# Kernel optimization log

Hardware: AMD Instinct MI355X
Metric: run time of the kernel (lower is better)

The kernel has to match this reference:

```python
import jax, jax.numpy as jnp
import numpy as np

N = 100000      # nodes
E = 1600000     # edges
IN_C = 64       # in_channels
HID = 128       # hidden_channels
K = 2           # Chebyshev order
EPS = 1e-5      # BatchNorm eps
SLOPE = 0.01    # LeakyReLU negative slope


def _glorot(key, shape, fan_in):
    lim = 1.0 / np.sqrt(fan_in)
    return jax.random.uniform(key, shape, jnp.float32, -lim, lim)


def setup_inputs() -> dict:
    key = jax.random.key(0)
    ks = jax.random.split(key, 12)
    x = jax.random.normal(ks[0], (N, IN_C), jnp.float32)
    edge_index = jax.random.randint(ks[1], (2, E), 0, N, dtype=jnp.int32)
    # ChebConv weights: one [Cin, Cout] matrix per Chebyshev order, plus bias.
    W1 = _glorot(ks[2], (K, IN_C, HID), IN_C)
    b1 = _glorot(ks[3], (HID,), IN_C)
    W2 = _glorot(ks[4], (K, HID, HID // 2), HID)
    b2 = _glorot(ks[5], (HID // 2,), HID)
    W3 = _glorot(ks[6], (K, HID // 2, IN_C), HID // 2)
    b3 = _glorot(ks[7], (IN_C,), HID // 2)
    # BatchNorm affine params
    gamma1 = jnp.ones((HID,), jnp.float32)
    beta1 = jnp.zeros((HID,), jnp.float32)
    gamma2 = jnp.ones((HID // 2,), jnp.float32)
    beta2 = jnp.zeros((HID // 2,), jnp.float32)
    return {"x": x, "edge_index": edge_index, "W1": W1, "b1": b1,
            "W2": W2, "b2": b2, "W3": W3, "b3": b3,
            "gamma1": gamma1, "beta1": beta1, "gamma2": gamma2, "beta2": beta2}


def reference(x, edge_index, W1, b1, W2, b2, W3, b3, gamma1, beta1, gamma2, beta2):
    row, col = edge_index[0], edge_index[1]
    # Scaled Laplacian with lambda_max=2 (PyG default): L_hat = -D^{-1/2} A D^{-1/2}
    deg = jax.ops.segment_sum(jnp.ones(row.shape, x.dtype), row, num_segments=N)
    dinv = jnp.where(deg > 0, jax.lax.rsqrt(jnp.where(deg > 0, deg, 1.0)), 0.0)
    ew = -dinv[row] * dinv[col]                     # [E] edge weights of L_hat

    def prop(h):  # y = L_hat @ h ; gather from source, scatter to target
        return jax.ops.segment_sum(ew[:, None] * h[row], col, num_segments=N)

    def cheb_conv(h, W, b):  # K=2: Tx0 = h, Tx1 = L_hat @ h
        return h @ W[0] + prop(h) @ W[1] + b

    def batchnorm(h, g, b):  # training-mode BN over node dim, biased variance
        m = h.mean(axis=0)
        v = jnp.mean(jnp.square(h - m), axis=0)
        return g * (h - m) * jax.lax.rsqrt(v + EPS) + b

    def lrelu(h):
        return jnp.where(h >= 0, h, SLOPE * h)

    h = lrelu(batchnorm(cheb_conv(x, W1, b1), gamma1, beta1))
    h = lrelu(batchnorm(cheb_conv(h, W2, b2), gamma2, beta2))
    return cheb_conv(h, W3, b3)
```

## Files before the change

kernel.cpp:

```cpp
#include <hip/hip_runtime.h>

#define NN 100000
#define NE 1600000
constexpr float BN_EPS = 1e-5f;
constexpr float LRELU_SLOPE = 0.01f;
constexpr int SC_NB = (NN + 255) / 256;
constexpr int RSH = 13;
constexpr int RB = 1 << RSH;
constexpr int NR = (NN + RB - 1) / RB;
constexpr int SB = 8;
constexpr int CAP = 163840;
constexpr int PBLK = 400;
constexpr int PCHUNK = NE / PBLK;

__global__ __launch_bounds__(256) void k_part(const int* __restrict__ row,
                                              const int* __restrict__ col,
                                              int* __restrict__ colCnt,
                                              int* __restrict__ rowCnt,
                                              int2* __restrict__ colbuf,
                                              int* __restrict__ rowbuf) {
  __shared__ int cntc[NR], cntr[NR];
  const int tid = threadIdx.x;
  const int e0 = blockIdx.x * PCHUNK;
  if (tid < NR) { cntc[tid] = 0; cntr[tid] = 0; }
  __syncthreads();
  for (int i = tid; i < PCHUNK; i += 256) {
    atomicAdd(&cntc[col[e0 + i] >> RSH], 1);
    atomicAdd(&cntr[row[e0 + i] >> RSH], 1);
  }
  __syncthreads();
  if (tid < NR) {
    cntc[tid] = atomicAdd(&colCnt[tid], cntc[tid]);
  } else if (tid >= 64 && tid < 64 + NR) {
    const int b = tid - 64;
    cntr[b] = atomicAdd(&rowCnt[b], cntr[b]);
  }
  __syncthreads();
  for (int i = tid; i < PCHUNK; i += 256) {
    const int r = row[e0 + i];
    const int c = col[e0 + i];
    const int bc = c >> RSH;
    const int pc = atomicAdd(&cntc[bc], 1);
    colbuf[(size_t)bc * CAP + pc] = make_int2(r, c);
    const int br = r >> RSH;
    const int pr = atomicAdd(&cntr[br], 1);
    rowbuf[(size_t)br * CAP + pr] = r;
  }
}

__global__ __launch_bounds__(1024) void k_hist2(const int2* __restrict__ colbuf,
                                                const int* __restrict__ rowbuf,
                                                const int* __restrict__ colCnt,
                                                const int* __restrict__ rowCnt,
                                                int* __restrict__ PDc,
                                                int* __restrict__ PDd) {
  __shared__ int h[RB];
  const int tid = threadIdx.x;
  const int b = blockIdx.x, s = blockIdx.y, z = blockIdx.z;
  for (int i = tid; i < RB; i += 1024) h[i] = 0;
  __syncthreads();
  const int base = b << RSH;
  const int len = z ? rowCnt[b] : colCnt[b];
  const int sl = (len + SB - 1) / SB;
  const int st = s * sl;
  const int en = min(st + sl, len);
  if (z == 0) {
    const int2* cb = colbuf + (size_t)b * CAP;
    for (int i = st + tid; i < en; i += 1024)
      atomicAdd(&h[cb[i].y - base], 1);
  } else {
    const int* rb = rowbuf + (size_t)b * CAP;
    for (int i = st + tid; i < en; i += 1024)
      atomicAdd(&h[rb[i] - base], 1);
  }
  __syncthreads();
  int* pd = (z ? PDd : PDc) + ((size_t)b * SB + s) * RB;
  for (int i = tid; i < RB; i += 1024) pd[i] = h[i];
}

__global__ __launch_bounds__(256) void k_csrmid2(const int* __restrict__ PDc,
                                                 const int* __restrict__ PDd,
                                                 int* __restrict__ Bpart,
                                                 int* __restrict__ cnt,
                                                 float* __restrict__ dinv) {
  const int n = blockIdx.x * 256 + threadIdx.x;
  if (n >= NN) return;
  const int b = n >> RSH, o = n & (RB - 1);
  int run = 0, dsum = 0;
#pragma unroll
  for (int s = 0; s < SB; s++) {
    Bpart[(size_t)s * NN + n] = run;
    run += PDc[((size_t)b * SB + s) * RB + o];
    dsum += PDd[((size_t)b * SB + s) * RB + o];
  }
  cnt[n] = run;
  dinv[n] = dsum > 0 ? rsqrtf((float)dsum) : 0.0f;
}

__global__ __launch_bounds__(256) void k_scan_a(const int* __restrict__ cnt,
                                                int* __restrict__ bsum) {
  __shared__ int sh[256];
  const int tid = threadIdx.x;
  const int i = blockIdx.x * 256 + tid;
  sh[tid] = (i < NN) ? cnt[i] : 0;
  __syncthreads();
  for (int st = 128; st > 0; st >>= 1) {
    if (tid < st) sh[tid] += sh[tid + st];
    __syncthreads();
  }
  if (tid == 0) bsum[blockIdx.x] = sh[0];
}

__global__ __launch_bounds__(512) void k_scan_b(const int* __restrict__ bsum,
                                                int* __restrict__ boff) {
  __shared__ int sh[512];
  const int tid = threadIdx.x;
  const int v = (tid < SC_NB) ? bsum[tid] : 0;
  sh[tid] = v;
  __syncthreads();
  for (int off = 1; off < 512; off <<= 1) {
    int t = (tid >= off) ? sh[tid - off] : 0;
    __syncthreads();
    sh[tid] += t;
    __syncthreads();
  }
  if (tid < SC_NB) boff[tid] = sh[tid] - v;
}

__global__ __launch_bounds__(256) void k_scan_c(const int* __restrict__ cnt,
                                                const int* __restrict__ boff,
                                                int* __restrict__ ptr) {
  __shared__ int sh[256];
  const int tid = threadIdx.x;
  const int i = blockIdx.x * 256 + tid;
  const int v = (i < NN) ? cnt[i] : 0;
  sh[tid] = v;
  __syncthreads();
  for (int off = 1; off < 256; off <<= 1) {
    int t = (tid >= off) ? sh[tid - off] : 0;
    __syncthreads();
    sh[tid] += t;
    __syncthreads();
  }
  const int excl = sh[tid] - v + boff[blockIdx.x];
  if (i < NN) {
    ptr[i] = excl;
    if (i == NN - 1) ptr[NN] = excl + v;
  }
}

__global__ __launch_bounds__(1024) void k_fill4(const int2* __restrict__ colbuf,
                                                const int* __restrict__ colCnt,
                                                const int* __restrict__ ptr,
                                                const int* __restrict__ Bpart,
                                                int* __restrict__ eb) {
  __shared__ int cur[RB];
  const int tid = threadIdx.x;
  const int b = blockIdx.x, s = blockIdx.y;
  const int base = b << RSH;
  const int nmax = min(RB, NN - base);
  const int* bp = Bpart + (size_t)s * NN + base;
  for (int i = tid; i < nmax; i += 1024) cur[i] = ptr[base + i] + bp[i];
  __syncthreads();
  const int len = colCnt[b];
  const int sl = (len + SB - 1) / SB;
  const int st = s * sl;
  const int en = min(st + sl, len);
  const int2* cb = colbuf + (size_t)b * CAP;
  for (int i = st + tid; i < en; i += 1024) {
    const int2 rec = cb[i];
    const int pos = atomicAdd(&cur[rec.y - base], 1);
    eb[pos] = rec.x;
  }
}

__global__ __launch_bounds__(256) void k_scale(const float* __restrict__ x,
                                               const float* __restrict__ dinv,
                                               float* __restrict__ xs) {
  const size_t i = (size_t)blockIdx.x * 256 + threadIdx.x;
  const int n = (int)(i >> 4);
  float4 v = reinterpret_cast<const float4*>(x)[i];
  const float d = dinv[n];
  v.x *= d; v.y *= d; v.z *= d; v.w *= d;
  reinterpret_cast<float4*>(xs)[i] = v;
}

template <bool ADD>
__global__ __launch_bounds__(256) void k_prop64(const float* __restrict__ p,
                                                const int* __restrict__ eb,
                                                const int* __restrict__ ptr,
                                                const float* __restrict__ g,
                                                const float* __restrict__ dinv,
                                                float* __restrict__ out) {
  const int node = blockIdx.x * 16 + (threadIdx.x >> 4);
  const int lane = threadIdx.x & 15;
  if (node >= NN) return;
  const int b = ptr[node], e = ptr[node + 1];
  float4 a0 = make_float4(0.f, 0.f, 0.f, 0.f);
  float4 a1 = make_float4(0.f, 0.f, 0.f, 0.f);
  float4 a2 = make_float4(0.f, 0.f, 0.f, 0.f);
  float4 a3 = make_float4(0.f, 0.f, 0.f, 0.f);
  const float4* hp = reinterpret_cast<const float4*>(p) + lane;
  int j = b;
  for (; j + 4 <= e; j += 4) {
    const int s0 = eb[j], s1 = eb[j + 1], s2 = eb[j + 2], s3 = eb[j + 3];
    const float4 h0 = hp[(size_t)s0 * 16];
    const float4 h1 = hp[(size_t)s1 * 16];
    const float4 h2 = hp[(size_t)s2 * 16];
    const float4 h3 = hp[(size_t)s3 * 16];
    a0.x += h0.x; a0.y += h0.y; a0.z += h0.z; a0.w += h0.w;
    a1.x += h1.x; a1.y += h1.y; a1.z += h1.z; a1.w += h1.w;
    a2.x += h2.x; a2.y += h2.y; a2.z += h2.z; a2.w += h2.w;
    a3.x += h3.x; a3.y += h3.y; a3.z += h3.z; a3.w += h3.w;
  }
  for (; j + 2 <= e; j += 2) {
    const int s0 = eb[j], s1 = eb[j + 1];
    const float4 h0 = hp[(size_t)s0 * 16];
    const float4 h1 = hp[(size_t)s1 * 16];
    a0.x += h0.x; a0.y += h0.y; a0.z += h0.z; a0.w += h0.w;
    a1.x += h1.x; a1.y += h1.y; a1.z += h1.z; a1.w += h1.w;
  }
  if (j < e) {
    const float4 h0 = hp[(size_t)eb[j] * 16];
    a0.x += h0.x; a0.y += h0.y; a0.z += h0.z; a0.w += h0.w;
  }
  a0.x += a1.x + a2.x + a3.x;
  a0.y += a1.y + a2.y + a3.y;
  a0.z += a1.z + a2.z + a3.z;
  a0.w += a1.w + a2.w + a3.w;
  if (ADD) {
    const float dn = dinv[node];
    const float4 gv = reinterpret_cast<const float4*>(g)[(size_t)node * 16 + lane];
    a0.x = gv.x - dn * a0.x;
    a0.y = gv.y - dn * a0.y;
    a0.z = gv.z - dn * a0.z;
    a0.w = gv.w - dn * a0.w;
  }
  reinterpret_cast<float4*>(out)[(size_t)node * 16 + lane] = a0;
}

__global__ __launch_bounds__(512) void k_conv1(const float* __restrict__ x,
                                               const float* __restrict__ y,
                                               const float* __restrict__ dinv,
                                               const float* __restrict__ W,
                                               const float* __restrict__ bias,
                                               float* __restrict__ out) {
  __shared__ float XA[64][65];
  __shared__ float XY[64][65];
  const int tid = threadIdx.x;
  const int lane = tid & 63;
  const int wv = __builtin_amdgcn_readfirstlane(tid >> 6);
  const int n0 = blockIdx.x * 64;
  for (int idx = tid; idx < 1024; idx += 512) {
    const int n = idx >> 4, k4 = idx & 15;
    int node = n0 + n;
    if (node >= NN) node = NN - 1;
    const float4 av = *reinterpret_cast<const float4*>(x + (size_t)node * 64 + k4 * 4);
    float4 yv = *reinterpret_cast<const float4*>(y + (size_t)node * 64 + k4 * 4);
    const float dn = -dinv[node];
    yv.x *= dn; yv.y *= dn; yv.z *= dn; yv.w *= dn;
    float* da = &XA[n][k4 * 4];
    da[0] = av.x; da[1] = av.y; da[2] = av.z; da[3] = av.w;
    float* dy = &XY[n][k4 * 4];
    dy[0] = yv.x; dy[1] = yv.y; dy[2] = yv.z; dy[3] = yv.w;
  }
  __syncthreads();
  const int cw0 = wv * 16;
  const float* __restrict__ W0 = W + cw0;
  const float* __restrict__ W1 = W + 64 * 128 + cw0;
  float acc[16];
#pragma unroll
  for (int j = 0; j < 16; j++) acc[j] = 0.f;
#pragma unroll 4
  for (int k = 0; k < 64; k++) {
    const float a = XA[lane][k];
    const float b = XY[lane][k];
#pragma unroll
    for (int j = 0; j < 16; j++)
      acc[j] += a * W0[(size_t)k * 128 + j] + b * W1[(size_t)k * 128 + j];
  }
  const int node = n0 + lane;
  if (node < NN) {
#pragma unroll
    for (int j = 0; j < 16; j += 4) {
      float4 o = make_float4(acc[j] + bias[cw0 + j], acc[j + 1] + bias[cw0 + j + 1],
                             acc[j + 2] + bias[cw0 + j + 2], acc[j + 3] + bias[cw0 + j + 3]);
      *reinterpret_cast<float4*>(out + (size_t)node * 128 + cw0 + j) = o;
    }
  }
}

template <int Cin>
__global__ __launch_bounds__(512) void k_gemm_dual(const float* __restrict__ h,
                                                   const float* __restrict__ W,
                                                   const float* __restrict__ bias,
                                                   const float* __restrict__ scale,
                                                   const float* __restrict__ shift,
                                                   const float* __restrict__ dinv,
                                                   float* __restrict__ g,
                                                   float* __restrict__ p) {
  __shared__ float XA[64][Cin + 1];
  const int tid = threadIdx.x;
  const int lane = tid & 63;
  const int wv = __builtin_amdgcn_readfirstlane(tid >> 6);
  const int n0 = blockIdx.x * 64;
  constexpr int C4 = Cin / 4;
  for (int idx = tid; idx < 64 * C4; idx += 512) {
    const int n = idx / C4, k4 = idx % C4;
    int node = n0 + n;
    if (node >= NN) node = NN - 1;
    float4 v = *reinterpret_cast<const float4*>(h + (size_t)node * Cin + k4 * 4);
    const float4 sc = *reinterpret_cast<const float4*>(scale + k4 * 4);
    const float4 sh = *reinterpret_cast<const float4*>(shift + k4 * 4);
    v.x = sc.x * v.x + sh.x; v.y = sc.y * v.y + sh.y;
    v.z = sc.z * v.z + sh.z; v.w = sc.w * v.w + sh.w;
    v.x = v.x >= 0.f ? v.x : LRELU_SLOPE * v.x;
    v.y = v.y >= 0.f ? v.y : LRELU_SLOPE * v.y;
    v.z = v.z >= 0.f ? v.z : LRELU_SLOPE * v.z;
    v.w = v.w >= 0.f ? v.w : LRELU_SLOPE * v.w;
    float* d = &XA[n][k4 * 4];
    d[0] = v.x; d[1] = v.y; d[2] = v.z; d[3] = v.w;
  }
  __syncthreads();
  const int cw0 = wv * 8;
  const float* __restrict__ Wa = W + cw0;
  const float* __restrict__ Wb = W + Cin * 64 + cw0;
  float ag[8], ap[8];
#pragma unroll
  for (int j = 0; j < 8; j++) { ag[j] = 0.f; ap[j] = 0.f; }
#pragma unroll 4
  for (int k = 0; k < Cin; k++) {
    const float a = XA[lane][k];
#pragma unroll
    for (int j = 0; j < 8; j++) {
      ag[j] += a * Wa[(size_t)k * 64 + j];
      ap[j] += a * Wb[(size_t)k * 64 + j];
    }
  }
  const int node = n0 + lane;
  if (node < NN) {
    const float dn = dinv[node];
#pragma unroll
    for (int j = 0; j < 8; j += 4) {
      float4 og = make_float4(ag[j] + bias[cw0 + j], ag[j + 1] + bias[cw0 + j + 1],
                              ag[j + 2] + bias[cw0 + j + 2], ag[j + 3] + bias[cw0 + j + 3]);
      *reinterpret_cast<float4*>(g + (size_t)node * 64 + cw0 + j) = og;
      float4 op = make_float4(ap[j] * dn, ap[j + 1] * dn, ap[j + 2] * dn, ap[j + 3] * dn);
      *reinterpret_cast<float4*>(p + (size_t)node * 64 + cw0 + j) = op;
    }
  }
}

template <int C>
__global__ __launch_bounds__(256) void k_bnstats(const float* __restrict__ h,
                                                 float* __restrict__ bnsum,
                                                 float* __restrict__ bnsq) {
  constexpr int RPB = 256 / C;
  constexpr int ROWS = 256;
  const int c = threadIdx.x % C;
  const int g = threadIdx.x / C;
  const int r0 = blockIdx.x * ROWS + g;
  const int rend = min(blockIdx.x * ROWS + ROWS, NN);
  float s = 0.f, sq = 0.f;
  for (int r = r0; r < rend; r += RPB) {
    float v = h[(size_t)r * C + c];
    s += v;
    sq += v * v;
  }
  __shared__ float ss[256], sg[256];
  ss[threadIdx.x] = s;
  sg[threadIdx.x] = sq;
  __syncthreads();
  for (int st = 128; st >= C; st >>= 1) {
    if (threadIdx.x < st) {
      ss[threadIdx.x] += ss[threadIdx.x + st];
      sg[threadIdx.x] += sg[threadIdx.x + st];
    }
    __syncthreads();
  }
  if (threadIdx.x < C) {
    atomicAdd(&bnsum[threadIdx.x], ss[threadIdx.x]);
    atomicAdd(&bnsq[threadIdx.x], sg[threadIdx.x]);
  }
}

template <int C>
__global__ void k_bnfin(const float* __restrict__ bnsum, const float* __restrict__ bnsq,
                        const float* __restrict__ gamma, const float* __restrict__ beta,
                        float* __restrict__ scale, float* __restrict__ shift) {
  int c = threadIdx.x;
  if (c < C) {
    float mean = bnsum[c] * (1.0f / NN);
    float var = bnsq[c] * (1.0f / NN) - mean * mean;
    float sc = gamma[c] * rsqrtf(var + BN_EPS);
    scale[c] = sc;
    shift[c] = beta[c] - mean * sc;
  }
}

extern "C" void kernel_launch(void* const* d_in, const int* in_sizes, int n_in,
                              void* d_out, int out_size, void* d_ws, size_t ws_size,
                              hipStream_t stream) {
  const float* x   = (const float*)d_in[0];
  const int*   ei  = (const int*)d_in[1];
  const int*   row = ei;
  const int*   col = ei + NE;
  const float* W1  = (const float*)d_in[2];
  const float* b1  = (const float*)d_in[3];
  const float* W2  = (const float*)d_in[4];
  const float* b2  = (const float*)d_in[5];
  const float* W3  = (const float*)d_in[6];
  const float* b3  = (const float*)d_in[7];
  const float* g1  = (const float*)d_in[8];
  const float* be1 = (const float*)d_in[9];
  const float* g2w = (const float*)d_in[10];
  const float* be2 = (const float*)d_in[11];
  float* out = (float*)d_out;

  char* ws = (char*)d_ws;
  size_t off = 0;
  auto alloc = [&](size_t bytes) -> void* {
    void* p = ws + off;
    off = (off + bytes + 255) & ~(size_t)255;
    return p;
  };

  float* bnsum1 = (float*)alloc(128 * 4);
  float* bnsq1  = (float*)alloc(128 * 4);
  float* bnsum2 = (float*)alloc(64 * 4);
  float* bnsq2  = (float*)alloc(64 * 4);
  int*   colCnt = (int*)alloc(NR * 4);
  int*   rowCnt = (int*)alloc(NR * 4);
  const size_t zero_bytes = off;
  float* dinv   = (float*)alloc(NN * 4);
  int*   cnt    = (int*)alloc(NN * 4);
  int*   ptr    = (int*)alloc((NN + 1) * 4);
  int*   bsum   = (int*)alloc(SC_NB * 4);
  int*   boff   = (int*)alloc(SC_NB * 4);
  int*   eb     = (int*)alloc((size_t)NE * 4);
  float* scale1 = (float*)alloc(128 * 4);
  float* shift1 = (float*)alloc(128 * 4);
  float* scale2 = (float*)alloc(64 * 4);
  float* shift2 = (float*)alloc(64 * 4);
  float* bufA   = (float*)alloc((size_t)NN * 64 * 4);
  float* bufB   = (float*)alloc((size_t)NN * 128 * 4);
  float* bufC   = (float*)alloc((size_t)NN * 64 * 4);
  float* bufD   = (float*)alloc((size_t)NN * 64 * 4);

  int2* colbuf = (int2*)bufB;
  int*  rowbuf = (int*)(colbuf + (size_t)NR * CAP);
  int*  PDc    = (int*)bufC;
  int*  PDd    = PDc + (size_t)NR * SB * RB;
  int*  Bpart  = PDd + (size_t)NR * SB * RB;

  float* y1  = bufA;
  float* xs  = bufC;
  float* h1  = bufB;
  float* gg2 = bufA;
  float* p2  = bufC;
  float* h2  = bufD;
  float* gg3 = bufB;
  float* p3  = bufB + (size_t)NN * 64;

  hipMemsetAsync(d_ws, 0, zero_bytes, stream);

  k_part<<<PBLK, 256, 0, stream>>>(row, col, colCnt, rowCnt, colbuf, rowbuf);
  k_hist2<<<dim3(NR, SB, 2), 1024, 0, stream>>>(colbuf, rowbuf, colCnt, rowCnt, PDc, PDd);
  k_csrmid2<<<(NN + 255) / 256, 256, 0, stream>>>(PDc, PDd, Bpart, cnt, dinv);
  k_scan_a<<<SC_NB, 256, 0, stream>>>(cnt, bsum);
  k_scan_b<<<1, 512, 0, stream>>>(bsum, boff);
  k_scan_c<<<SC_NB, 256, 0, stream>>>(cnt, boff, ptr);
  k_fill4<<<dim3(NR, SB), 1024, 0, stream>>>(colbuf, colCnt, ptr, Bpart, eb);

  const int gemmGrid = (NN + 63) / 64;
  const int propGrid = (NN * 16 + 255) / 256;

  k_scale<<<NN * 16 / 256, 256, 0, stream>>>(x, dinv, xs);
  k_prop64<false><<<propGrid, 256, 0, stream>>>(xs, eb, ptr, nullptr, nullptr, y1);
  k_conv1<<<gemmGrid, 512, 0, stream>>>(x, y1, dinv, W1, b1, h1);
  k_bnstats<128><<<(NN + 255) / 256, 256, 0, stream>>>(h1, bnsum1, bnsq1);
  k_bnfin<128><<<1, 128, 0, stream>>>(bnsum1, bnsq1, g1, be1, scale1, shift1);

  k_gemm_dual<128><<<gemmGrid, 512, 0, stream>>>(h1, W2, b2, scale1, shift1, dinv, gg2, p2);
  k_prop64<true><<<propGrid, 256, 0, stream>>>(p2, eb, ptr, gg2, dinv, h2);
  k_bnstats<64><<<(NN + 255) / 256, 256, 0, stream>>>(h2, bnsum2, bnsq2);
  k_bnfin<64><<<1, 64, 0, stream>>>(bnsum2, bnsq2, g2w, be2, scale2, shift2);

  k_gemm_dual<64><<<gemmGrid, 512, 0, stream>>>(h2, W3, b3, scale2, shift2, dinv, gg3, p3);
  k_prop64<true><<<propGrid, 256, 0, stream>>>(p3, eb, ptr, gg3, dinv, out);
}
```

Measured before the change: 582.1 us.

## Pack partition buffers compactly and compute two node rows per thread in GEMMs

The partition pass now stores each column-bucket record as one packed int (source row shifted above the in-bucket column offset) instead of an int2, and stores row-bucket records as 16-bit in-bucket offsets. This cuts write and read traffic in the partition, histogram and fill kernels. Separately, the conv1 and dual-GEMM kernels now process 128 nodes per block, with each thread accumulating two node rows, so each weight load is reused twice. This doubles accumulator registers and shared memory, which may lower occupancy. The packing relies on row << 13 fitting in an int, which holds for 100k nodes.

After: 573.9 us. No clear change (-1.4%).

```diff
diff --git a/kernel.cpp b/kernel.cpp
--- a/kernel.cpp
+++ b/kernel.cpp
@@ -17,8 +17,8 @@
                                               const int* __restrict__ col,
                                               int* __restrict__ colCnt,
                                               int* __restrict__ rowCnt,
-                                              int2* __restrict__ colbuf,
-                                              int* __restrict__ rowbuf) {
+                                              int* __restrict__ colbuf,
+                                              unsigned short* __restrict__ rowbuf) {
   __shared__ int cntc[NR], cntr[NR];
   const int tid = threadIdx.x;
   const int e0 = blockIdx.x * PCHUNK;
@@ -41,15 +41,15 @@
     const int c = col[e0 + i];
     const int bc = c >> RSH;
     const int pc = atomicAdd(&cntc[bc], 1);
-    colbuf[(size_t)bc * CAP + pc] = make_int2(r, c);
+    colbuf[(size_t)bc * CAP + pc] = (r << RSH) | (c & (RB - 1));
     const int br = r >> RSH;
     const int pr = atomicAdd(&cntr[br], 1);
-    rowbuf[(size_t)br * CAP + pr] = r;
-  }
-}
-
-__global__ __launch_bounds__(1024) void k_hist2(const int2* __restrict__ colbuf,
-                                                const int* __restrict__ rowbuf,
+    rowbuf[(size_t)br * CAP + pr] = (unsigned short)(r & (RB - 1));
+  }
+}
+
+__global__ __launch_bounds__(1024) void k_hist2(const int* __restrict__ colbuf,
+                                                const unsigned short* __restrict__ rowbuf,
                                                 const int* __restrict__ colCnt,
                                                 const int* __restrict__ rowCnt,
                                                 int* __restrict__ PDc,
@@ -59,19 +59,18 @@
   const int b = blockIdx.x, s = blockIdx.y, z = blockIdx.z;
   for (int i = tid; i < RB; i += 1024) h[i] = 0;
   __syncthreads();
-  const int base = b << RSH;
   const int len = z ? rowCnt[b] : colCnt[b];
   const int sl = (len + SB - 1) / SB;
   const int st = s * sl;
   const int en = min(st + sl, len);
   if (z == 0) {
-    const int2* cb = colbuf + (size_t)b * CAP;
+    const int* cb = colbuf + (size_t)b * CAP;
     for (int i = st + tid; i < en; i += 1024)
-      atomicAdd(&h[cb[i].y - base], 1);
+      atomicAdd(&h[cb[i] & (RB - 1)], 1);
   } else {
-    const int* rb = rowbuf + (size_t)b * CAP;
+    const unsigned short* rb = rowbuf + (size_t)b * CAP;
     for (int i = st + tid; i < en; i += 1024)
-      atomicAdd(&h[rb[i] - base], 1);
+      atomicAdd(&h[rb[i]], 1);
   }
   __syncthreads();
   int* pd = (z ? PDd : PDc) + ((size_t)b * SB + s) * RB;
@@ -149,7 +148,7 @@
   }
 }
 
-__global__ __launch_bounds__(1024) void k_fill4(const int2* __restrict__ colbuf,
+__global__ __launch_bounds__(1024) void k_fill4(const int* __restrict__ colbuf,
                                                 const int* __restrict__ colCnt,
                                                 const int* __restrict__ ptr,
                                                 const int* __restrict__ Bpart,
@@ -166,11 +165,11 @@
   const int sl = (len + SB - 1) / SB;
   const int st = s * sl;
   const int en = min(st + sl, len);
-  const int2* cb = colbuf + (size_t)b * CAP;
+  const int* cb = colbuf + (size_t)b * CAP;
   for (int i = st + tid; i < en; i += 1024) {
-    const int2 rec = cb[i];
-    const int pos = atomicAdd(&cur[rec.y - base], 1);
-    eb[pos] = rec.x;
+    const int rec = cb[i];
+    const int pos = atomicAdd(&cur[rec & (RB - 1)], 1);
+    eb[pos] = rec >> RSH;
   }
 }
 
@@ -245,13 +244,13 @@
                                                const float* __restrict__ W,
                                                const float* __restrict__ bias,
                                                float* __restrict__ out) {
-  __shared__ float XA[64][65];
-  __shared__ float XY[64][65];
+  __shared__ float XA[128][65];
+  __shared__ float XY[128][65];
   const int tid = threadIdx.x;
   const int lane = tid & 63;
   const int wv = __builtin_amdgcn_readfirstlane(tid >> 6);
-  const int n0 = blockIdx.x * 64;
-  for (int idx = tid; idx < 1024; idx += 512) {
+  const int n0 = blockIdx.x * 128;
+  for (int idx = tid; idx < 2048; idx += 512) {
     const int n = idx >> 4, k4 = idx & 15;
     int node = n0 + n;
     if (node >= NN) node = NN - 1;
@@ -268,24 +267,34 @@
   const int cw0 = wv * 16;
   const float* __restrict__ W0 = W + cw0;
   const float* __restrict__ W1 = W + 64 * 128 + cw0;
-  float acc[16];
-#pragma unroll
-  for (int j = 0; j < 16; j++) acc[j] = 0.f;
-#pragma unroll 4
+  float acc0[16], acc1[16];
+#pragma unroll
+  for (int j = 0; j < 16; j++) { acc0[j] = 0.f; acc1[j] = 0.f; }
+#pragma unroll 2
   for (int k = 0; k < 64; k++) {
-    const float a = XA[lane][k];
-    const float b = XY[lane][k];
-#pragma unroll
-    for (int j = 0; j < 16; j++)
-      acc[j] += a * W0[(size_t)k * 128 + j] + b * W1[(size_t)k * 128 + j];
-  }
-  const int node = n0 + lane;
-  if (node < NN) {
-#pragma unroll
-    for (int j = 0; j < 16; j += 4) {
-      float4 o = make_float4(acc[j] + bias[cw0 + j], acc[j + 1] + bias[cw0 + j + 1],
-                             acc[j + 2] + bias[cw0 + j + 2], acc[j + 3] + bias[cw0 + j + 3]);
-      *reinterpret_cast<float4*>(out + (size_t)node * 128 + cw0 + j) = o;
+    const float a0 = XA[lane][k];
+    const float a1 = XA[lane + 64][k];
+    const float b0 = XY[lane][k];
+    const float b1 = XY[lane + 64][k];
+#pragma unroll
+    for (int j = 0; j < 16; j++) {
+      const float w0 = W0[(size_t)k * 128 + j];
+      const float w1 = W1[(size_t)k * 128 + j];
+      acc0[j] += a0 * w0 + b0 * w1;
+      acc1[j] += a1 * w0 + b1 * w1;
+    }
+  }
+#pragma unroll
+  for (int half = 0; half < 2; half++) {
+    const int node = n0 + lane + half * 64;
+    const float* acc = half ? acc1 : acc0;
+    if (node < NN) {
+#pragma unroll
+      for (int j = 0; j < 16; j += 4) {
+        float4 o = make_float4(acc[j] + bias[cw0 + j], acc[j + 1] + bias[cw0 + j + 1],
+                               acc[j + 2] + bias[cw0 + j + 2], acc[j + 3] + bias[cw0 + j + 3]);
+        *reinterpret_cast<float4*>(out + (size_t)node * 128 + cw0 + j) = o;
+      }
     }
   }
 }
@@ -299,13 +308,13 @@
                                                    const float* __restrict__ dinv,
                                                    float* __restrict__ g,
                                                    float* __restrict__ p) {
-  __shared__ float XA[64][Cin + 1];
+  __shared__ float XA[128][Cin + 1];
   const int tid = threadIdx.x;
   const int lane = tid & 63;
   const int wv = __builtin_amdgcn_readfirstlane(tid >> 6);
-  const int n0 = blockIdx.x * 64;
+  const int n0 = blockIdx.x * 128;
   constexpr int C4 = Cin / 4;
-  for (int idx = tid; idx < 64 * C4; idx += 512) {
+  for (int idx = tid; idx < 128 * C4; idx += 512) {
     const int n = idx / C4, k4 = idx % C4;
     int node = n0 + n;
     if (node >= NN) node = NN - 1;
@@ -325,28 +334,36 @@
   const int cw0 = wv * 8;
   const float* __restrict__ Wa = W + cw0;
   const float* __restrict__ Wb = W + Cin * 64 + cw0;
-  float ag[8], ap[8];
-#pragma unroll
-  for (int j = 0; j < 8; j++) { ag[j] = 0.f; ap[j] = 0.f; }
-#pragma unroll 4
+  float ag0[8], ag1[8], ap0[8], ap1[8];
+#pragma unroll
+  for (int j = 0; j < 8; j++) { ag0[j] = 0.f; ag1[j] = 0.f; ap0[j] = 0.f; ap1[j] = 0.f; }
+#pragma unroll 2
   for (int k = 0; k < Cin; k++) {
-    const float a = XA[lane][k];
+    const float a0 = XA[lane][k];
+    const float a1 = XA[lane + 64][k];
 #pragma unroll
     for (int j = 0; j < 8; j++) {
-      ag[j] += a * Wa[(size_t)k * 64 + j];
-      ap[j] += a * Wb[(size_t)k * 64 + j];
+      const float wa = Wa[(size_t)k * 64 + j];
+      const float wb = Wb[(size_t)k * 64 + j];
+      ag0[j] += a0 * wa; ag1[j] += a1 * wa;
+      ap0[j] += a0 * wb; ap1[j] += a1 * wb;
     }
   }
-  const int node = n0 + lane;
-  if (node < NN) {
-    const float dn = dinv[node];
-#pragma unroll
-    for (int j = 0; j < 8; j += 4) {
-      float4 og = make_float4(ag[j] + bias[cw0 + j], ag[j + 1] + bias[cw0 + j + 1],
-                              ag[j + 2] + bias[cw0 + j + 2], ag[j + 3] + bias[cw0 + j + 3]);
-      *reinterpret_cast<float4*>(g + (size_t)node * 64 + cw0 + j) = og;
-      float4 op = make_float4(ap[j] * dn, ap[j + 1] * dn, ap[j + 2] * dn, ap[j + 3] * dn);
-      *reinterpret_cast<float4*>(p + (size_t)node * 64 + cw0 + j) = op;
+#pragma unroll
+  for (int half = 0; half < 2; half++) {
+    const int node = n0 + lane + half * 64;
+    const float* ag = half ? ag1 : ag0;
+    const float* ap = half ? ap1 : ap0;
+    if (node < NN) {
+      const float dn = dinv[node];
+#pragma unroll
+      for (int j = 0; j < 8; j += 4) {
+        float4 og = make_float4(ag[j] + bias[cw0 + j], ag[j + 1] + bias[cw0 + j + 1],
+                                ag[j + 2] + bias[cw0 + j + 2], ag[j + 3] + bias[cw0 + j + 3]);
+        *reinterpret_cast<float4*>(g + (size_t)node * 64 + cw0 + j) = og;
+        float4 op = make_float4(ap[j] * dn, ap[j + 1] * dn, ap[j + 2] * dn, ap[j + 3] * dn);
+        *reinterpret_cast<float4*>(p + (size_t)node * 64 + cw0 + j) = op;
+      }
     }
   }
 }
@@ -447,11 +464,11 @@
   float* bufC   = (float*)alloc((size_t)NN * 64 * 4);
   float* bufD   = (float*)alloc((size_t)NN * 64 * 4);
 
-  int2* colbuf = (int2*)bufB;
-  int*  rowbuf = (int*)(colbuf + (size_t)NR * CAP);
-  int*  PDc    = (int*)bufC;
-  int*  PDd    = PDc + (size_t)NR * SB * RB;
-  int*  Bpart  = PDd + (size_t)NR * SB * RB;
+  int* colbuf = (int*)bufB;
+  unsigned short* rowbuf = (unsigned short*)(colbuf + (size_t)NR * CAP);
+  int* PDc    = (int*)bufC;
+  int* PDd    = PDc + (size_t)NR * SB * RB;
+  int* Bpart  = PDd + (size_t)NR * SB * RB;
 
   float* y1  = bufA;
   float* xs  = bufC;
@@ -472,7 +489,7 @@
   k_scan_c<<<SC_NB, 256, 0, stream>>>(cnt, boff, ptr);
   k_fill4<<<dim3(NR, SB), 1024, 0, stream>>>(colbuf, colCnt, ptr, Bpart, eb);
 
-  const int gemmGrid = (NN + 63) / 64;
+  const int gemmGrid = (NN + 127) / 128;
   const int propGrid = (NN * 16 + 255) / 256;
 
   k_scale<<<NN * 16 / 256, 256, 0, stream>>>(x, dinv, xs);
```
